# Kernel tuning notes

Hardware: AMD Instinct MI355X
Metric: run time of the kernel (lower is better)

Reference implementation:

```python
import jax, jax.numpy as jnp
import numpy as np

D = 1024
H = 16
HD = D // H
FF = 4 * D
EPS = 1e-5


def _layernorm(x, g, s):
    m = x.mean(-1, keepdims=True)
    v = ((x - m) ** 2).mean(-1, keepdims=True)  # unbiased=False
    return g * (x - m) / jnp.sqrt(v + EPS) + s


def _gelu_tanh(x):
    c = jnp.sqrt(2.0 / jnp.pi).astype(x.dtype)
    return 0.5 * x * (1 + jnp.tanh(c * (x + 0.044715 * x ** 3)))


def setup_inputs() -> dict:
    key = jax.random.key(0)
    ks = jax.random.split(key, 12)
    B, T = 2, 2048
    std = 0.02
    x = jax.random.normal(ks[0], (B, T, D), jnp.float32)
    wq = jax.random.normal(ks[1], (D, D), jnp.float32) * std
    wk = jax.random.normal(ks[2], (D, D), jnp.float32) * std
    wv = jax.random.normal(ks[3], (D, D), jnp.float32) * std
    wo = jax.random.normal(ks[4], (D, D), jnp.float32) * std
    bo = jnp.zeros((D,), jnp.float32)
    w1 = jax.random.normal(ks[5], (FF, D), jnp.float32) * std
    b1 = jnp.zeros((FF,), jnp.float32)
    w2 = jax.random.normal(ks[6], (D, FF), jnp.float32) * std
    b2 = jnp.zeros((D,), jnp.float32)
    g1 = jnp.ones((D,), jnp.float32)
    s1 = jnp.zeros((D,), jnp.float32)
    g2 = jnp.ones((D,), jnp.float32)
    s2 = jnp.zeros((D,), jnp.float32)
    return {"x": x, "wq": wq, "wk": wk, "wv": wv, "wo": wo, "bo": bo,
            "w1": w1, "b1": b1, "w2": w2, "b2": b2,
            "g1": g1, "s1": s1, "g2": g2, "s2": s2}


def reference(x, wq, wk, wv, wo, bo, w1, b1, w2, b2, g1, s1, g2, s2):
    B, T, _ = x.shape
    # pre-LN attention
    h = _layernorm(x, g1, s1)
    q = (h @ wq.T).reshape(B, T, H, HD).transpose(0, 2, 1, 3)  # [B,H,T,HD]
    k = (h @ wk.T).reshape(B, T, H, HD).transpose(0, 2, 1, 3)
    v = (h @ wv.T).reshape(B, T, H, HD).transpose(0, 2, 1, 3)
    scores = jnp.einsum('bhqd,bhkd->bhqk', q, k)
    causal = jnp.triu(jnp.ones((T, T), bool), k=1)
    scores = jnp.where(causal, -jnp.inf, scores)
    attn = jax.nn.softmax(scores / jnp.sqrt(jnp.float32(HD)), axis=-1)
    ctx = jnp.einsum('bhqk,bhkd->bhqd', attn, v)
    ctx = ctx.transpose(0, 2, 1, 3).reshape(B, T, D)
    x = x + (ctx @ wo.T + bo)
    # pre-LN MLP
    h2 = _layernorm(x, g2, s2)
    ff = _gelu_tanh(h2 @ w1.T + b1) @ w2.T + b2
    return x + ff
```

## Files before the change

### kernel.cpp

```cpp
#include <hip/hip_runtime.h>
#include <hip/hip_bf16.h>
#include <stdint.h>


typedef __attribute__((ext_vector_type(8))) __bf16 bf16x8;
typedef __attribute__((ext_vector_type(4))) __bf16 bf16x4;
typedef __attribute__((ext_vector_type(4))) float  f32x4;

#define DD    1024
#define TSEQ  2048
#define NTOK  4096
#define FFD   4096

#define ASM_VMCNT4() asm volatile("s_waitcnt vmcnt(4)" ::: "memory")
#define ASM_VMCNT0() asm volatile("s_waitcnt vmcnt(0)" ::: "memory")
#define ASM_LGKM0()  asm volatile("s_waitcnt lgkmcnt(0)" ::: "memory")

__device__ __forceinline__ void gll16(const void* g, void* l) {
  __builtin_amdgcn_global_load_lds(
      (const __attribute__((address_space(1))) unsigned int*)g,
      (__attribute__((address_space(3))) unsigned int*)l, 16, 0, 0);
}

__device__ __forceinline__ float gelu_f(float v) {
  float u = 0.7978845608028654f * (v + 0.044715f * v * v * v);
  float t = 1.0f - 2.0f / (1.0f + __expf(2.0f * u));
  return 0.5f * v * (1.0f + t);
}

__global__ __launch_bounds__(256) void cvt_weights(
    const float* __restrict__ wq, const float* __restrict__ wk,
    const float* __restrict__ wv, const float* __restrict__ wo,
    const float* __restrict__ w1, const float* __restrict__ w2,
    __bf16* __restrict__ dst)
{
  size_t i4 = (size_t)blockIdx.x * 256 + threadIdx.x;
  size_t e = i4 * 4;
  const float* src; size_t off;
  if (e < (size_t)4 * 1048576) {
    int sel = (int)(e >> 20);
    src = sel == 0 ? wq : sel == 1 ? wk : sel == 2 ? wv : wo;
    off = e & 1048575;
  } else if (e < (size_t)8 * 1048576) {
    src = w1; off = e - (size_t)4 * 1048576;
  } else {
    src = w2; off = e - (size_t)8 * 1048576;
  }
  float4 v = *(const float4*)(src + off);
  bf16x4 o;
  o[0] = (__bf16)v.x; o[1] = (__bf16)v.y; o[2] = (__bf16)v.z; o[3] = (__bf16)v.w;
  *(bf16x4*)(dst + e) = o;
}

__global__ __launch_bounds__(256) void ln_kernel(
    const float* __restrict__ x, const float* __restrict__ gw,
    const float* __restrict__ sw, __bf16* __restrict__ out)
{
  const int row  = blockIdx.x * 4 + (threadIdx.x >> 6);
  const int lane = threadIdx.x & 63;
  const float4* xr = (const float4*)(x + (size_t)row * DD);
  float4 v[4];
  float s = 0.f, sq = 0.f;
#pragma unroll
  for (int i = 0; i < 4; ++i) {
    v[i] = xr[i * 64 + lane];
    s  += v[i].x + v[i].y + v[i].z + v[i].w;
    sq += v[i].x * v[i].x + v[i].y * v[i].y + v[i].z * v[i].z + v[i].w * v[i].w;
  }
#pragma unroll
  for (int off = 32; off >= 1; off >>= 1) {
    s  += __shfl_xor(s, off);
    sq += __shfl_xor(sq, off);
  }
  const float mean = s * (1.f / DD);
  const float rstd = rsqrtf(sq * (1.f / DD) - mean * mean + 1e-5f);
  const float4* gr = (const float4*)gw;
  const float4* sr = (const float4*)sw;
#pragma unroll
  for (int i = 0; i < 4; ++i) {
    float4 gv = gr[i * 64 + lane];
    float4 sv = sr[i * 64 + lane];
    bf16x4 o;
    o[0] = (__bf16)(gv.x * (v[i].x - mean) * rstd + sv.x);
    o[1] = (__bf16)(gv.y * (v[i].y - mean) * rstd + sv.y);
    o[2] = (__bf16)(gv.z * (v[i].z - mean) * rstd + sv.z);
    o[3] = (__bf16)(gv.w * (v[i].w - mean) * rstd + sv.w);
    *(bf16x4*)&out[(size_t)row * DD + (size_t)(i * 64 + lane) * 4] = o;
  }
}

template<int MODE>
__global__ __launch_bounds__(512, 2)
void gemm256(const __bf16* __restrict__ A, int lda,
             const __bf16* __restrict__ Bw, int ldb,
             __bf16* __restrict__ Cout, const float* __restrict__ bias,
             __bf16* __restrict__ voutT, int M, int N, int K)
{
  __shared__ __bf16 sm[65536];
  const int t = threadIdx.x;
  const int lane = t & 63;
  const int l15 = lane & 15, g = lane >> 4;
  const int w = t >> 6;
  const int wm = w >> 2, wn = w & 3;
  const int m0 = blockIdx.y * 256, n0 = blockIdx.x * 256;

  if (MODE == 2) {
    const int kz = blockIdx.z;
    A    += (size_t)kz * 1024;
    Bw   += (size_t)kz * 1024;
    Cout += (size_t)kz * (size_t)M * N;
  }

  auto STAGE_A = [&](int kt, int h, int b) {
#pragma unroll
    for (int i = 0; i < 2; ++i) {
      const int slot = i * 512 + t;
      const int row  = h * 128 + (slot >> 3);
      const int gc   = (slot & 7) ^ (row & 7);
      gll16(A + (size_t)(m0 + row) * lda + kt * 64 + gc * 8,
            sm + b * 32768 + h * 8192 + slot * 8);
    }
  };
  auto STAGE_B = [&](int kt, int h, int b) {
#pragma unroll
    for (int i = 0; i < 2; ++i) {
      const int slot = i * 512 + t;
      const int row  = h * 128 + (slot >> 3);
      const int gc   = (slot & 7) ^ (row & 7);
      gll16(Bw + (size_t)(n0 + row) * ldb + kt * 64 + gc * 8,
            sm + b * 32768 + 16384 + h * 8192 + slot * 8);
    }
  };

  f32x4 acc[8][4] = {};
  const int NT = K >> 6;

  STAGE_A(0, 0, 0); STAGE_A(0, 1, 0);
  STAGE_B(0, 0, 0); STAGE_B(0, 1, 0);
  STAGE_B(1, 0, 1); STAGE_B(1, 1, 1);
  ASM_VMCNT4();
  __builtin_amdgcn_s_barrier();

  for (int kt = 0; kt < NT; ++kt) {
    const int cb = kt & 1;
    const __bf16* sA = sm + cb * 32768;
    const __bf16* sB = sm + cb * 32768 + 16384;
    const bool pf1 = (kt + 1 < NT);
    const bool pf2 = (kt + 2 < NT);

    bf16x8 afl[4][2], afh[4][2], bfl[2][2], bfh[2][2];

#pragma unroll
    for (int mi = 0; mi < 4; ++mi) {
      const int row = wm * 128 + mi * 16 + l15;
#pragma unroll
      for (int ks = 0; ks < 2; ++ks)
        afl[mi][ks] = *(const bf16x8*)&sA[row * 64 + (((ks * 4 + g) ^ (row & 7)) * 8)];
    }
#pragma unroll
    for (int ni = 0; ni < 2; ++ni) {
      const int row = wn * 64 + ni * 16 + l15;
#pragma unroll
      for (int ks = 0; ks < 2; ++ks)
        bfl[ni][ks] = *(const bf16x8*)&sB[row * 64 + (((ks * 4 + g) ^ (row & 7)) * 8)];
    }
    if (pf1) STAGE_A(kt + 1, 0, cb ^ 1);
    __builtin_amdgcn_s_barrier();
    ASM_LGKM0();
    __builtin_amdgcn_sched_barrier(0);
    __builtin_amdgcn_s_setprio(1);
#pragma unroll
    for (int ks = 0; ks < 2; ++ks)
#pragma unroll
      for (int mi = 0; mi < 4; ++mi)
#pragma unroll
        for (int ni = 0; ni < 2; ++ni)
          acc[mi][ni] = __builtin_amdgcn_mfma_f32_16x16x32_bf16(
              afl[mi][ks], bfl[ni][ks], acc[mi][ni], 0, 0, 0);
    __builtin_amdgcn_s_setprio(0);
    __builtin_amdgcn_s_barrier();

#pragma unroll
    for (int ni = 0; ni < 2; ++ni) {
      const int row = wn * 64 + (ni + 2) * 16 + l15;
#pragma unroll
      for (int ks = 0; ks < 2; ++ks)
        bfh[ni][ks] = *(const bf16x8*)&sB[row * 64 + (((ks * 4 + g) ^ (row & 7)) * 8)];
    }
    if (pf1) STAGE_A(kt + 1, 1, cb ^ 1);
    __builtin_amdgcn_s_barrier();
    ASM_LGKM0();
    __builtin_amdgcn_sched_barrier(0);
    __builtin_amdgcn_s_setprio(1);
#pragma unroll
    for (int ks = 0; ks < 2; ++ks)
#pragma unroll
      for (int mi = 0; mi < 4; ++mi)
#pragma unroll
        for (int ni = 0; ni < 2; ++ni)
          acc[mi][ni + 2] = __builtin_amdgcn_mfma_f32_16x16x32_bf16(
              afl[mi][ks], bfh[ni][ks], acc[mi][ni + 2], 0, 0, 0);
    __builtin_amdgcn_s_setprio(0);
    __builtin_amdgcn_s_barrier();

#pragma unroll
    for (int mi = 0; mi < 4; ++mi) {
      const int row = wm * 128 + (mi + 4) * 16 + l15;
#pragma unroll
      for (int ks = 0; ks < 2; ++ks)
        afh[mi][ks] = *(const bf16x8*)&sA[row * 64 + (((ks * 4 + g) ^ (row & 7)) * 8)];
    }
    if (pf2) STAGE_B(kt + 2, 0, cb);
    __builtin_amdgcn_s_barrier();
    ASM_LGKM0();
    __builtin_amdgcn_sched_barrier(0);
    __builtin_amdgcn_s_setprio(1);
#pragma unroll
    for (int ks = 0; ks < 2; ++ks)
#pragma unroll
      for (int mi = 0; mi < 4; ++mi)
#pragma unroll
        for (int ni = 0; ni < 2; ++ni)
          acc[mi + 4][ni + 2] = __builtin_amdgcn_mfma_f32_16x16x32_bf16(
              afh[mi][ks], bfh[ni][ks], acc[mi + 4][ni + 2], 0, 0, 0);
    __builtin_amdgcn_s_setprio(0);
    __builtin_amdgcn_s_barrier();

    if (pf2) STAGE_B(kt + 2, 1, cb);
    __builtin_amdgcn_s_barrier();
    __builtin_amdgcn_s_setprio(1);
#pragma unroll
    for (int ks = 0; ks < 2; ++ks)
#pragma unroll
      for (int mi = 0; mi < 4; ++mi)
#pragma unroll
        for (int ni = 0; ni < 2; ++ni)
          acc[mi + 4][ni] = __builtin_amdgcn_mfma_f32_16x16x32_bf16(
              afh[mi][ks], bfl[ni][ks], acc[mi + 4][ni], 0, 0, 0);
    __builtin_amdgcn_s_setprio(0);
    if (pf1) { if (pf2) ASM_VMCNT4(); else ASM_VMCNT0(); }
    __builtin_amdgcn_s_barrier();
  }

#pragma unroll
  for (int mi = 0; mi < 8; ++mi) {
    const int rr0 = m0 + wm * 128 + mi * 16 + 4 * g;
#pragma unroll
    for (int ni = 0; ni < 4; ++ni) {
      const int cc = n0 + wn * 64 + ni * 16 + l15;
      if (MODE == 0 && n0 + wn * 64 >= 2048) {
        const int b  = rr0 >> 11;
        const int t0 = rr0 & 2047;
        const int vc = cc - 2048;
        const int h = vc >> 6, d = vc & 63;
        bf16x4 o;
        o[0] = (__bf16)acc[mi][ni][0]; o[1] = (__bf16)acc[mi][ni][1];
        o[2] = (__bf16)acc[mi][ni][2]; o[3] = (__bf16)acc[mi][ni][3];
        *(bf16x4*)&voutT[(((size_t)(b * 16 + h)) * 64 + d) * 2048 + t0] = o;
      } else {
        const int ldc = (MODE == 0) ? 2048 : N;
#pragma unroll
        for (int r = 0; r < 4; ++r) {
          float v = acc[mi][ni][r];
          if (MODE == 1) { v += bias[cc]; v = gelu_f(v); }
          Cout[(size_t)(rr0 + r) * ldc + cc] = (__bf16)v;
        }
      }
    }
  }
}

__global__ __launch_bounds__(256) void ff2_reduce(
    const __bf16* __restrict__ part, const float* __restrict__ x2,
    const float* __restrict__ b2, float* __restrict__ out)
{
  const size_t e = ((size_t)blockIdx.x * 256 + threadIdx.x) * 4;
  float4 r = *(const float4*)(x2 + e);
  const float4 b = *(const float4*)(b2 + (e & 1023));
  r.x += b.x; r.y += b.y; r.z += b.z; r.w += b.w;
#pragma unroll
  for (int s = 0; s < 4; ++s) {
    bf16x4 p = *(const bf16x4*)(part + (size_t)s * 4194304 + e);
    r.x += (float)p[0]; r.y += (float)p[1]; r.z += (float)p[2]; r.w += (float)p[3];
  }
  *(float4*)(out + e) = r;
}

template<bool BIAS, bool RES>
__global__ __launch_bounds__(256, 3)
void gemm_bt(const __bf16* __restrict__ A, const __bf16* __restrict__ Bw,
             float* __restrict__ Cout, const float* __restrict__ bias,
             const float* __restrict__ res, int M, int N, int K)
{
  __shared__ __bf16 As[128 * 64];
  __shared__ __bf16 Bs[128 * 64];
  const int t    = threadIdx.x;
  const int lane = t & 63;
  const int l15  = lane & 15;
  const int g    = lane >> 4;
  const int w    = t >> 6;
  const int wr   = w >> 1, wc = w & 1;
  const int m0 = blockIdx.y * 128;
  const int n0 = blockIdx.x * 128;
  const int srow = t >> 3;
  const int scol = (t & 7) * 8;

  f32x4 acc[4][4] = {};
  const __bf16* Ap = A  + (size_t)m0 * K;
  const __bf16* Bp = Bw + (size_t)n0 * K;

  for (int k0 = 0; k0 < K; k0 += 64) {
#pragma unroll
    for (int i = 0; i < 4; ++i) {
      const int row = i * 32 + srow;
      gll16(Ap + (size_t)row * K + k0 + scol, &As[row * 64 + scol]);
    }
#pragma unroll
    for (int i = 0; i < 4; ++i) {
      const int row = i * 32 + srow;
      gll16(Bp + (size_t)row * K + k0 + scol, &Bs[row * 64 + scol]);
    }
    __syncthreads();
#pragma unroll
    for (int ks = 0; ks < 2; ++ks) {
      bf16x8 af[4], bfr[4];
#pragma unroll
      for (int mi = 0; mi < 4; ++mi)
        af[mi] = *(const bf16x8*)&As[(wr * 64 + mi * 16 + l15) * 64 + ks * 32 + g * 8];
#pragma unroll
      for (int ni = 0; ni < 4; ++ni)
        bfr[ni] = *(const bf16x8*)&Bs[(wc * 64 + ni * 16 + l15) * 64 + ks * 32 + g * 8];
#pragma unroll
      for (int mi = 0; mi < 4; ++mi)
#pragma unroll
        for (int ni = 0; ni < 4; ++ni)
          acc[mi][ni] = __builtin_amdgcn_mfma_f32_16x16x32_bf16(af[mi], bfr[ni], acc[mi][ni], 0, 0, 0);
    }
    __syncthreads();
  }

  const int crow0 = m0 + wr * 64;
  const int ccol0 = n0 + wc * 64;
#pragma unroll
  for (int mi = 0; mi < 4; ++mi) {
#pragma unroll
    for (int r = 0; r < 4; ++r) {
      const int rr = crow0 + mi * 16 + 4 * g + r;
#pragma unroll
      for (int ni = 0; ni < 4; ++ni) {
        const int cc = ccol0 + ni * 16 + l15;
        float v = acc[mi][ni][r];
        if (BIAS) v += bias[cc];
        if (RES)  v += res[(size_t)rr * N + cc];
        Cout[(size_t)rr * N + cc] = v;
      }
    }
  }
}

__global__ __launch_bounds__(256, 2)
void attn_kernel(const __bf16* __restrict__ qk, const __bf16* __restrict__ vT,
                 __bf16* __restrict__ ctx)
{
  __shared__ __bf16 Ks[64][72];
  __shared__ __bf16 VTs[64][72];
  __shared__ __bf16 Ps[4][16][72];
  const int t    = threadIdx.x;
  const int lane = t & 63;
  const int l15  = lane & 15;
  const int g    = lane >> 4;
  const int w    = t >> 6;
  const int qt = gridDim.x - 1 - blockIdx.x;
  const int hh = blockIdx.y;
  const int bb = blockIdx.z;
  const int q0 = qt * 64;

  const int qrow = q0 + w * 16 + l15;
  const size_t qkrow = ((size_t)(bb * 2048 + qrow)) * 2048 + hh * 64;
  bf16x8 qf[2];
  qf[0] = *(const bf16x8*)&qk[qkrow + g * 8];
  qf[1] = *(const bf16x8*)&qk[qkrow + 32 + g * 8];

  f32x4 acc[4] = {};
  float mrun = -1e30f, lrun = 0.f;

  for (int kt = 0; kt <= qt; ++kt) {
    __syncthreads();
    {
      const int kk = t >> 2;
      const int d0 = (t & 3) * 16;
      const __bf16* krow = &qk[((size_t)(bb * 2048 + kt * 64 + kk)) * 2048 + 1024 + hh * 64];
      *(bf16x8*)&Ks[kk][d0]     = *(const bf16x8*)&krow[d0];
      *(bf16x8*)&Ks[kk][d0 + 8] = *(const bf16x8*)&krow[d0 + 8];
      const __bf16* vrow = &vT[(((size_t)(bb * 16 + hh)) * 64 + kk) * 2048 + kt * 64 + d0];
      *(bf16x8*)&VTs[kk][d0]     = *(const bf16x8*)&vrow[0];
      *(bf16x8*)&VTs[kk][d0 + 8] = *(const bf16x8*)&vrow[8];
    }
    __syncthreads();

    f32x4 s[4];
#pragma unroll
    for (int f = 0; f < 4; ++f) {
      f32x4 z = {};
      bf16x8 a0 = *(const bf16x8*)&Ks[f * 16 + l15][g * 8];
      bf16x8 a1 = *(const bf16x8*)&Ks[f * 16 + l15][32 + g * 8];
      z = __builtin_amdgcn_mfma_f32_16x16x32_bf16(a0, qf[0], z, 0, 0, 0);
      z = __builtin_amdgcn_mfma_f32_16x16x32_bf16(a1, qf[1], z, 0, 0, 0);
      s[f] = z;
    }

    const int qg = q0 + w * 16 + l15;
    float pmax = -1e30f;
#pragma unroll
    for (int f = 0; f < 4; ++f)
#pragma unroll
      for (int r = 0; r < 4; ++r) {
        float sv = s[f][r] * 0.125f;
        const int kg = kt * 64 + f * 16 + g * 4 + r;
        if (kg > qg) sv = -1e30f;
        s[f][r] = sv;
        pmax = fmaxf(pmax, sv);
      }
    pmax = fmaxf(pmax, __shfl_xor(pmax, 16));
    pmax = fmaxf(pmax, __shfl_xor(pmax, 32));
    const float mnew  = fmaxf(mrun, pmax);
    const float alpha = __expf(mrun - mnew);
    float lsum = 0.f;
#pragma unroll
    for (int f = 0; f < 4; ++f)
#pragma unroll
      for (int r = 0; r < 4; ++r) {
        float p = __expf(s[f][r] - mnew);
        s[f][r] = p;
        lsum += p;
      }
    lsum += __shfl_xor(lsum, 16);
    lsum += __shfl_xor(lsum, 32);
    lrun = lrun * alpha + lsum;
    mrun = mnew;

#pragma unroll
    for (int f = 0; f < 4; ++f) {
      bf16x4 pk;
      pk[0] = (__bf16)s[f][0]; pk[1] = (__bf16)s[f][1];
      pk[2] = (__bf16)s[f][2]; pk[3] = (__bf16)s[f][3];
      *(bf16x4*)&Ps[w][l15][f * 16 + g * 4] = pk;
    }
    asm volatile("s_waitcnt lgkmcnt(0)" ::: "memory");

    float al[4];
#pragma unroll
    for (int r = 0; r < 4; ++r) al[r] = __shfl(alpha, g * 4 + r);
#pragma unroll
    for (int nf = 0; nf < 4; ++nf)
#pragma unroll
      for (int r = 0; r < 4; ++r) acc[nf][r] *= al[r];

#pragma unroll
    for (int ks = 0; ks < 2; ++ks) {
      bf16x8 pa = *(const bf16x8*)&Ps[w][l15][ks * 32 + g * 8];
#pragma unroll
      for (int nf = 0; nf < 4; ++nf) {
        bf16x8 vf = *(const bf16x8*)&VTs[nf * 16 + l15][ks * 32 + g * 8];
        acc[nf] = __builtin_amdgcn_mfma_f32_16x16x32_bf16(pa, vf, acc[nf], 0, 0, 0);
      }
    }
  }

  float li[4];
#pragma unroll
  for (int r = 0; r < 4; ++r) li[r] = 1.0f / __shfl(lrun, g * 4 + r);
#pragma unroll
  for (int nf = 0; nf < 4; ++nf)
#pragma unroll
    for (int r = 0; r < 4; ++r) {
      const int row = q0 + w * 16 + 4 * g + r;
      ctx[((size_t)(bb * 2048 + row)) * DD + hh * 64 + nf * 16 + l15] =
          (__bf16)(acc[nf][r] * li[r]);
    }
}

extern "C" void kernel_launch(void* const* d_in, const int* in_sizes, int n_in,
                              void* d_out, int out_size, void* d_ws, size_t ws_size,
                              hipStream_t stream)
{
  (void)in_sizes; (void)n_in; (void)out_size; (void)ws_size;
  const float* x  = (const float*)d_in[0];
  const float* wq = (const float*)d_in[1];
  const float* wk = (const float*)d_in[2];
  const float* wv = (const float*)d_in[3];
  const float* wo = (const float*)d_in[4];
  const float* bo = (const float*)d_in[5];
  const float* w1 = (const float*)d_in[6];
  const float* b1 = (const float*)d_in[7];
  const float* w2 = (const float*)d_in[8];
  const float* b2 = (const float*)d_in[9];
  const float* g1 = (const float*)d_in[10];
  const float* s1 = (const float*)d_in[11];
  const float* g2 = (const float*)d_in[12];
  const float* s2 = (const float*)d_in[13];
  float* out = (float*)d_out;

  char* ws = (char*)d_ws;
  __bf16* wbf  = (__bf16*)ws;
  __bf16* hbuf = (__bf16*)(ws + 25165824);
  __bf16* qkb  = (__bf16*)(ws + 33554432);
  __bf16* vbT  = (__bf16*)(ws + 50331648);
  __bf16* ctxb = (__bf16*)(ws + 58720256);
  float*  x2   = (float*)(ws + 67108864);
  __bf16* ffb  = (__bf16*)(ws + 83886080);
  __bf16* part = (__bf16*)(ws + 33554432);

  cvt_weights<<<12288, 256, 0, stream>>>(wq, wk, wv, wo, w1, w2, wbf);
  ln_kernel<<<1024, 256, 0, stream>>>(x, g1, s1, hbuf);

  gemm256<0><<<dim3(12, 16), 512, 0, stream>>>(
      hbuf, 1024, wbf, 1024, qkb, nullptr, vbT, NTOK, 3072, 1024);

  dim3 ga(32, 16, 2);
  attn_kernel<<<ga, 256, 0, stream>>>(qkb, vbT, ctxb);

  gemm_bt<true, true><<<dim3(8, 32), 256, 0, stream>>>(
      ctxb, wbf + 3145728, x2, bo, x, NTOK, DD, DD);
  ln_kernel<<<1024, 256, 0, stream>>>(x2, g2, s2, hbuf);

  gemm256<1><<<dim3(16, 16), 512, 0, stream>>>(
      hbuf, 1024, wbf + 4194304, 1024, ffb, b1, nullptr, NTOK, FFD, 1024);

  gemm256<2><<<dim3(4, 16, 4), 512, 0, stream>>>(
      ffb, 4096, wbf + 8388608, 4096, part, nullptr, nullptr, NTOK, DD, 1024);
  ff2_reduce<<<4096, 256, 0, stream>>>(part, x2, b2, out);
}
```

Baseline: 266.4 us.

## Prefetch K/V tiles into registers, swizzle LDS, and skip redundant softmax work

The attention kernel now prefetches the next K/V tile into registers while computing the current one, using ping-pong register sets, so global load latency overlaps compute. Padded LDS arrays are replaced by XOR-swizzled 128-byte rows to avoid bank conflicts without padding. The causal mask is applied only on the diagonal tile, and accumulator rescaling is skipped when no running max changes. The 1/sqrt(d) scale is folded into the Q projection epilogue. The costs are more registers under the (256,2) launch bound and a vmcnt(0) wait that may still serialize loads.

```diff
diff --git a/kernel.cpp b/kernel.cpp
--- a/kernel.cpp
+++ b/kernel.cpp
@@ -262,6 +262,7 @@
 #pragma unroll
         for (int r = 0; r < 4; ++r) {
           float v = acc[mi][ni][r];
+          if (MODE == 0 && cc < 1024) v *= 0.125f;
           if (MODE == 1) { v += bias[cc]; v = gelu_f(v); }
           Cout[(size_t)(rr0 + r) * ldc + cc] = (__bf16)v;
         }
@@ -362,9 +363,9 @@
 void attn_kernel(const __bf16* __restrict__ qk, const __bf16* __restrict__ vT,
                  __bf16* __restrict__ ctx)
 {
-  __shared__ __bf16 Ks[64][72];
-  __shared__ __bf16 VTs[64][72];
-  __shared__ __bf16 Ps[4][16][72];
+  __shared__ __bf16 Ks[64 * 64];
+  __shared__ __bf16 VTs[64 * 64];
+  __shared__ __bf16 Ps[4][16 * 64];
   const int t    = threadIdx.x;
   const int lane = t & 63;
   const int l15  = lane & 15;
@@ -377,94 +378,141 @@
 
   const int qrow = q0 + w * 16 + l15;
   const size_t qkrow = ((size_t)(bb * 2048 + qrow)) * 2048 + hh * 64;
-  bf16x8 qf[2];
-  qf[0] = *(const bf16x8*)&qk[qkrow + g * 8];
-  qf[1] = *(const bf16x8*)&qk[qkrow + 32 + g * 8];
+  bf16x8 qf0 = *(const bf16x8*)&qk[qkrow + g * 8];
+  bf16x8 qf1 = *(const bf16x8*)&qk[qkrow + 32 + g * 8];
+
+  const int kk = t >> 2;
+  const int c0 = (t & 3) * 16;
+  const __bf16* kbase = &qk[((size_t)(bb * 2048) + kk) * 2048 + 1024 + hh * 64 + c0];
+  const __bf16* vbase = &vT[(((size_t)(bb * 16 + hh)) * 64 + kk) * 2048 + c0];
+  const int xw  = (kk & 7) << 4;
+  char* kdst = (char*)Ks  + kk * 128;
+  char* vdst = (char*)VTs + kk * 128;
+  const int cw0 = ((((t & 3) * 2)    ) << 4) ^ xw;
+  const int cw1 = ((((t & 3) * 2) + 1) << 4) ^ xw;
 
   f32x4 acc[4] = {};
   float mrun = -1e30f, lrun = 0.f;
 
-  for (int kt = 0; kt <= qt; ++kt) {
-    __syncthreads();
-    {
-      const int kk = t >> 2;
-      const int d0 = (t & 3) * 16;
-      const __bf16* krow = &qk[((size_t)(bb * 2048 + kt * 64 + kk)) * 2048 + 1024 + hh * 64];
-      *(bf16x8*)&Ks[kk][d0]     = *(const bf16x8*)&krow[d0];
-      *(bf16x8*)&Ks[kk][d0 + 8] = *(const bf16x8*)&krow[d0 + 8];
-      const __bf16* vrow = &vT[(((size_t)(bb * 16 + hh)) * 64 + kk) * 2048 + kt * 64 + d0];
-      *(bf16x8*)&VTs[kk][d0]     = *(const bf16x8*)&vrow[0];
-      *(bf16x8*)&VTs[kk][d0 + 8] = *(const bf16x8*)&vrow[8];
-    }
-    __syncthreads();
-
+  bf16x8 ka0, ka1, va0, va1, kb0, kb1, vb0, vb1;
+
+  auto LOAD = [&](int kt, bf16x8& k0, bf16x8& k1, bf16x8& v0, bf16x8& v1) {
+    const __bf16* kp = kbase + (size_t)kt * 64 * 2048;
+    k0 = *(const bf16x8*)(kp);
+    k1 = *(const bf16x8*)(kp + 8);
+    const __bf16* vp = vbase + kt * 64;
+    v0 = *(const bf16x8*)(vp);
+    v1 = *(const bf16x8*)(vp + 8);
+  };
+  auto WRITE = [&](bf16x8& k0, bf16x8& k1, bf16x8& v0, bf16x8& v1) {
+    *(bf16x8*)(kdst + cw0) = k0;
+    *(bf16x8*)(kdst + cw1) = k1;
+    *(bf16x8*)(vdst + cw0) = v0;
+    *(bf16x8*)(vdst + cw1) = v1;
+  };
+
+  const int xr = (l15 & 7) << 4;
+  char* pw = (char*)Ps[w] + l15 * 128;
+
+  auto COMPUTE = [&](int kt) {
     f32x4 s[4];
 #pragma unroll
     for (int f = 0; f < 4; ++f) {
+      const char* kb = (const char*)Ks + (f * 16 + l15) * 128;
+      bf16x8 a0 = *(const bf16x8*)(kb + ((g << 4) ^ xr));
+      bf16x8 a1 = *(const bf16x8*)(kb + (((4 + g) << 4) ^ xr));
       f32x4 z = {};
-      bf16x8 a0 = *(const bf16x8*)&Ks[f * 16 + l15][g * 8];
-      bf16x8 a1 = *(const bf16x8*)&Ks[f * 16 + l15][32 + g * 8];
-      z = __builtin_amdgcn_mfma_f32_16x16x32_bf16(a0, qf[0], z, 0, 0, 0);
-      z = __builtin_amdgcn_mfma_f32_16x16x32_bf16(a1, qf[1], z, 0, 0, 0);
+      z = __builtin_amdgcn_mfma_f32_16x16x32_bf16(a0, qf0, z, 0, 0, 0);
+      z = __builtin_amdgcn_mfma_f32_16x16x32_bf16(a1, qf1, z, 0, 0, 0);
       s[f] = z;
     }
 
-    const int qg = q0 + w * 16 + l15;
     float pmax = -1e30f;
-#pragma unroll
-    for (int f = 0; f < 4; ++f)
-#pragma unroll
-      for (int r = 0; r < 4; ++r) {
-        float sv = s[f][r] * 0.125f;
-        const int kg = kt * 64 + f * 16 + g * 4 + r;
-        if (kg > qg) sv = -1e30f;
-        s[f][r] = sv;
-        pmax = fmaxf(pmax, sv);
-      }
+    if (kt == qt) {
+      const int qg = q0 + w * 16 + l15;
+#pragma unroll
+      for (int f = 0; f < 4; ++f)
+#pragma unroll
+        for (int r = 0; r < 4; ++r) {
+          const int kg = kt * 64 + f * 16 + g * 4 + r;
+          if (kg > qg) s[f][r] = -1e30f;
+          pmax = fmaxf(pmax, s[f][r]);
+        }
+    } else {
+#pragma unroll
+      for (int f = 0; f < 4; ++f)
+#pragma unroll
+        for (int r = 0; r < 4; ++r) pmax = fmaxf(pmax, s[f][r]);
+    }
     pmax = fmaxf(pmax, __shfl_xor(pmax, 16));
     pmax = fmaxf(pmax, __shfl_xor(pmax, 32));
-    const float mnew  = fmaxf(mrun, pmax);
-    const float alpha = __expf(mrun - mnew);
+
+    if (__any(pmax > mrun)) {
+      const float mnew  = fmaxf(mrun, pmax);
+      const float alpha = __expf(mrun - mnew);
+      float al[4];
+#pragma unroll
+      for (int r = 0; r < 4; ++r) al[r] = __shfl(alpha, g * 4 + r);
+#pragma unroll
+      for (int nf = 0; nf < 4; ++nf)
+#pragma unroll
+        for (int r = 0; r < 4; ++r) acc[nf][r] *= al[r];
+      lrun *= alpha;
+      mrun = mnew;
+    }
+
     float lsum = 0.f;
 #pragma unroll
     for (int f = 0; f < 4; ++f)
 #pragma unroll
       for (int r = 0; r < 4; ++r) {
-        float p = __expf(s[f][r] - mnew);
+        float p = __expf(s[f][r] - mrun);
         s[f][r] = p;
         lsum += p;
       }
     lsum += __shfl_xor(lsum, 16);
     lsum += __shfl_xor(lsum, 32);
-    lrun = lrun * alpha + lsum;
-    mrun = mnew;
+    lrun += lsum;
 
 #pragma unroll
     for (int f = 0; f < 4; ++f) {
       bf16x4 pk;
       pk[0] = (__bf16)s[f][0]; pk[1] = (__bf16)s[f][1];
       pk[2] = (__bf16)s[f][2]; pk[3] = (__bf16)s[f][3];
-      *(bf16x4*)&Ps[w][l15][f * 16 + g * 4] = pk;
+      *(bf16x4*)(pw + ((((f * 2 + (g >> 1)) << 4) ^ xr) + (g & 1) * 8)) = pk;
     }
     asm volatile("s_waitcnt lgkmcnt(0)" ::: "memory");
 
-    float al[4];
-#pragma unroll
-    for (int r = 0; r < 4; ++r) al[r] = __shfl(alpha, g * 4 + r);
-#pragma unroll
-    for (int nf = 0; nf < 4; ++nf)
-#pragma unroll
-      for (int r = 0; r < 4; ++r) acc[nf][r] *= al[r];
-
 #pragma unroll
     for (int ks = 0; ks < 2; ++ks) {
-      bf16x8 pa = *(const bf16x8*)&Ps[w][l15][ks * 32 + g * 8];
+      bf16x8 pa = *(const bf16x8*)(pw + (((ks * 4 + g) << 4) ^ xr));
 #pragma unroll
       for (int nf = 0; nf < 4; ++nf) {
-        bf16x8 vf = *(const bf16x8*)&VTs[nf * 16 + l15][ks * 32 + g * 8];
+        const char* vb = (const char*)VTs + (nf * 16 + l15) * 128;
+        bf16x8 vf = *(const bf16x8*)(vb + (((ks * 4 + g) << 4) ^ xr));
         acc[nf] = __builtin_amdgcn_mfma_f32_16x16x32_bf16(pa, vf, acc[nf], 0, 0, 0);
       }
     }
+  };
+
+  LOAD(0, ka0, ka1, va0, va1);
+  int kt = 0;
+  for (;;) {
+    ASM_VMCNT0();
+    __syncthreads();
+    WRITE(ka0, ka1, va0, va1);
+    if (kt < qt) LOAD(kt + 1, kb0, kb1, vb0, vb1);
+    __syncthreads();
+    COMPUTE(kt);
+    if (++kt > qt) break;
+
+    ASM_VMCNT0();
+    __syncthreads();
+    WRITE(kb0, kb1, vb0, vb1);
+    if (kt < qt) LOAD(kt + 1, ka0, ka1, va0, va1);
+    __syncthreads();
+    COMPUTE(kt);
+    if (++kt > qt) break;
   }
 
   float li[4];
```

Result: faster. 241.8 us (-9.2%).
